# Performance work log

Measured on AMD Instinct MI355X. Metric: run time of the kernel, lower is better.

Reference implementation:

```python
import jax, jax.numpy as jnp
import numpy as np

B, S, D, H, F = 2, 2048, 1024, 16, 4096
HD = D // H
EPS = 1e-5


def setup_inputs() -> dict:
    key = jax.random.key(0)
    ks = jax.random.split(key, 12)
    sc = 0.02
    inp = {
        "feature": jax.random.normal(ks[0], (B, S, D), jnp.float32),
        "src_key_padding_mask": jnp.ones((B, S), bool),
        # torch Linear weights stored as [in, out] (already transposed)
        "wq": jax.random.normal(ks[1], (D, D), jnp.float32) * sc,
        "bq": jnp.zeros((D,), jnp.float32),
        "wk": jax.random.normal(ks[2], (D, D), jnp.float32) * sc,
        "bk": jnp.zeros((D,), jnp.float32),
        "wv": jax.random.normal(ks[3], (D, D), jnp.float32) * sc,
        "bv": jnp.zeros((D,), jnp.float32),
        "wo": jax.random.normal(ks[4], (D, D), jnp.float32) * sc,
        "bo": jnp.zeros((D,), jnp.float32),
        "ln1_g": jnp.ones((D,), jnp.float32),
        "ln1_b": jnp.zeros((D,), jnp.float32),
        "ln2_g": jnp.ones((D,), jnp.float32),
        "ln2_b": jnp.zeros((D,), jnp.float32),
        "w1": jax.random.normal(ks[5], (D, F), jnp.float32) * sc,
        "b1": jnp.zeros((F,), jnp.float32),
        "w2": jax.random.normal(ks[6], (F, D), jnp.float32) * sc,
        "b2": jnp.zeros((D,), jnp.float32),
    }
    return inp


def _layer_norm(x, g, b):
    mu = jnp.mean(x, axis=-1, keepdims=True)
    var = jnp.mean(jnp.square(x - mu), axis=-1, keepdims=True)
    return (x - mu) * jax.lax.rsqrt(var + EPS) * g + b


def _encoder_layer(feature, san_mask, wq, bq, wk, bk, wv, bv, wo, bo,
                   ln1_g, ln1_b, ln2_g, ln2_b, w1, b1, w2, b2):
    # pre-norm (_forward_prenorm), dropout = 0 (eval)
    residual = feature
    x = _layer_norm(feature, ln1_g, ln1_b)
    q = (x @ wq + bq).reshape(B, S, H, HD)
    k = (x @ wk + bk).reshape(B, S, H, HD)
    v = (x @ wv + bv).reshape(B, S, H, HD)
    scale = jnp.float32(np.sqrt(HD))
    scores = jnp.einsum('bihd,bjhd->bhij', q, k) / scale  # [B,H,S,S]
    neg_inf = jnp.finfo(scores.dtype).min
    if san_mask is not None:
        scores = jnp.where(san_mask[:, None, :, :], scores, neg_inf)
    attw = jax.nn.softmax(scores, axis=-1)
    cvec = jnp.einsum('bhij,bjhd->bihd', attw, v).reshape(B, S, D)
    feature = cvec @ wo + bo + residual
    residual = feature
    x = _layer_norm(feature, ln2_g, ln2_b)
    x = jax.nn.gelu(x @ w1 + b1, approximate=False) @ w2 + b2
    return x + residual


def reference(feature, src_key_padding_mask, wq, bq, wk, bk, wv, bv, wo, bo,
              ln1_g, ln1_b, ln2_g, ln2_b, w1, b1, w2, b2):
    # make_san_mask: pad_mask [B,S] -> [B,S(q),S(k)] (no causal mask)
    san_mask = jnp.broadcast_to(src_key_padding_mask[:, None, :], (B, S, S))
    return _encoder_layer(feature, san_mask, wq, bq, wk, bk, wv, bv, wo, bo,
                          ln1_g, ln1_b, ln2_g, ln2_b, w1, b1, w2, b2)
```

## Files before the change

kernel.cpp:

```cpp
#include <hip/hip_runtime.h>
#include <hip/hip_bf16.h>
#include <math.h>

#define BB   2
#define SS   2048
#define DD   1024
#define HH   16
#define HDIM 64
#define FF   4096

typedef __hip_bfloat16 bf16_t;
typedef short s8v __attribute__((ext_vector_type(8)));
typedef float f4v __attribute__((ext_vector_type(4)));

#define PSTRIDE 4194304

__device__ inline unsigned bfr(float x) {
    unsigned u = __float_as_uint(x);
    return (u + 0x7fffu + ((u >> 16) & 1u)) >> 16;
}
__device__ inline unsigned bfpack(float lo, float hi) {
    return bfr(lo) | (bfr(hi) << 16);
}
__device__ inline float bflo(unsigned u) { return __uint_as_float(u << 16); }
__device__ inline float bfhi(unsigned u) { return __uint_as_float(u & 0xffff0000u); }
__device__ inline void gload16(const void* g, void* l) {
    __builtin_amdgcn_global_load_lds(
        (const __attribute__((address_space(1))) void*)g,
        (__attribute__((address_space(3))) void*)l, 16, 0, 0);
}

__global__ __launch_bounds__(256) void wtrans_all(
    const float* __restrict__ wq, const float* __restrict__ wk,
    const float* __restrict__ wv, const float* __restrict__ wo,
    const float* __restrict__ w1, const float* __restrict__ w2,
    bf16_t* __restrict__ dqkv, bf16_t* __restrict__ dwo,
    bf16_t* __restrict__ dw1, bf16_t* __restrict__ dw2) {
    __shared__ float tile[32][33];
    int id = blockIdx.x;
    const float* src; bf16_t* dst; int K, N, n0, k0;
    if (id < 4096) {
        int seg = id >> 10, r = id & 1023;
        K = 1024; N = 1024; n0 = (r & 31) * 32; k0 = (r >> 5) * 32;
        if (seg == 0)      { src = wq; dst = dqkv; }
        else if (seg == 1) { src = wk; dst = dqkv + 1024 * 1024; }
        else if (seg == 2) { src = wv; dst = dqkv + 2 * 1024 * 1024; }
        else               { src = wo; dst = dwo; }
    } else if (id < 8192) {
        int r = id - 4096;
        K = 1024; N = 4096; n0 = (r & 127) * 32; k0 = (r >> 7) * 32;
        src = w1; dst = dw1;
    } else {
        int r = id - 8192;
        K = 4096; N = 1024; n0 = (r & 31) * 32; k0 = (r >> 5) * 32;
        src = w2; dst = dw2;
    }
    int tx = threadIdx.x, ty = threadIdx.y;
#pragma unroll
    for (int i = 0; i < 4; i++)
        tile[ty * 4 + i][tx] = src[(size_t)(k0 + ty * 4 + i) * N + n0 + tx];
    __syncthreads();
#pragma unroll
    for (int i = 0; i < 4; i++) {
        unsigned short h = (unsigned short)bfr(tile[tx][ty * 4 + i]);
        *(unsigned short*)&dst[(size_t)(n0 + ty * 4 + i) * K + k0 + tx] = h;
    }
}

__global__ __launch_bounds__(256) void ln_k(const float* __restrict__ x,
                                            const float* __restrict__ gam,
                                            const float* __restrict__ bet,
                                            bf16_t* __restrict__ out) {
    int row = blockIdx.x, t = threadIdx.x;
    const float4 v = *(const float4*)&x[(size_t)row * DD + t * 4];
    float s  = v.x + v.y + v.z + v.w;
    float s2 = v.x * v.x + v.y * v.y + v.z * v.z + v.w * v.w;
#pragma unroll
    for (int off = 1; off < 64; off <<= 1) {
        s  += __shfl_xor(s, off);
        s2 += __shfl_xor(s2, off);
    }
    __shared__ float sb[8];
    int w = t >> 6, lane = t & 63;
    if (lane == 0) { sb[w] = s; sb[4 + w] = s2; }
    __syncthreads();
    s  = sb[0] + sb[1] + sb[2] + sb[3];
    s2 = sb[4] + sb[5] + sb[6] + sb[7];
    float mu  = s * (1.f / DD);
    float var = s2 * (1.f / DD) - mu * mu;
    float rs  = rsqrtf(var + 1e-5f);
    float4 gv = *(const float4*)&gam[t * 4];
    float4 bv = *(const float4*)&bet[t * 4];
    float o0 = (v.x - mu) * rs * gv.x + bv.x;
    float o1 = (v.y - mu) * rs * gv.y + bv.y;
    float o2 = (v.z - mu) * rs * gv.z + bv.z;
    float o3 = (v.w - mu) * rs * gv.w + bv.w;
    uint2 uu; uu.x = bfpack(o0, o1); uu.y = bfpack(o2, o3);
    *(uint2*)&out[(size_t)row * DD + t * 4] = uu;
}

template <int MODE, int SPLITS, int SWIZ>
__global__ __launch_bounds__(256, 2) void gemm_bt(
    const bf16_t* __restrict__ A, const bf16_t* __restrict__ Bt,
    int M, int N, int K,
    const float* __restrict__ bias0, const float* __restrict__ bias1,
    const float* __restrict__ bias2, const float* __restrict__ resid,
    float* __restrict__ outF,
    bf16_t* __restrict__ o0, bf16_t* __restrict__ o1, bf16_t* __restrict__ o2) {
    __shared__ bf16_t As[128 * 64];
    __shared__ bf16_t Bs[128 * 64];
    const int t = threadIdx.x;
    const int lane = t & 63, w = t >> 6;
    const int c = lane & 15, g = lane >> 4;
    const int wm = w & 1, wn = w >> 1;

    int bx, by, z;
    if (SWIZ == 0) { bx = blockIdx.x; by = blockIdx.y; z = blockIdx.z; }
    else if (SWIZ == 1) {
        int b = blockIdx.x, xcd = b & 7, j = b >> 3;
        by = xcd * 4 + (j & 3); bx = j >> 2; z = 0;
    } else {
        int b = blockIdx.x, xcd = b & 7, j = b >> 3;
        z = xcd >> 1; by = (xcd & 1) * 16 + (j & 15); bx = j >> 4;
    }
    const int m0 = by * 128, n0 = bx * 128;

    f4v acc[4][4];
#pragma unroll
    for (int i = 0; i < 4; i++)
#pragma unroll
        for (int j = 0; j < 4; j++)
#pragma unroll
            for (int r = 0; r < 4; r++) acc[i][j][r] = 0.f;

    const int row0 = t >> 3;
    const int kk   = (((t & 7) ^ (row0 & 7)) << 3);
    const bf16_t* ga = A  + (size_t)(m0 + row0) * K + kk;
    const bf16_t* gb = Bt + (size_t)(n0 + row0) * K + kk;

    const int fs0 = ((g)     ^ (c & 7)) * 8;
    const int fs1 = ((4 + g) ^ (c & 7)) * 8;
    int kbeg = 0, kend = K;
    if (MODE == 3) { kbeg = z * (K / SPLITS); kend = kbeg + (K / SPLITS); }

    for (int k0 = kbeg; k0 < kend; k0 += 64) {
        __syncthreads();
#pragma unroll
        for (int p = 0; p < 4; p++) {
            gload16(ga + k0 + (size_t)(32 * p) * K, &As[p * 2048 + t * 8]);
            gload16(gb + k0 + (size_t)(32 * p) * K, &Bs[p * 2048 + t * 8]);
        }
        __syncthreads();
#pragma unroll
        for (int kh = 0; kh < 2; kh++) {
            const int fs = kh ? fs1 : fs0;
            s8v af[4], bfg[4];
#pragma unroll
            for (int mi = 0; mi < 4; mi++)
                af[mi] = *(const s8v*)&As[(wm * 64 + mi * 16 + c) * 64 + fs];
#pragma unroll
            for (int ni = 0; ni < 4; ni++)
                bfg[ni] = *(const s8v*)&Bs[(wn * 64 + ni * 16 + c) * 64 + fs];
#pragma unroll
            for (int mi = 0; mi < 4; mi++)
#pragma unroll
                for (int ni = 0; ni < 4; ni++)
                    acc[mi][ni] = __builtin_amdgcn_mfma_f32_16x16x32_bf16(
                        af[mi], bfg[ni], acc[mi][ni], 0, 0, 0);
        }
    }

#pragma unroll
    for (int mi = 0; mi < 4; mi++) {
        int m = m0 + wm * 64 + mi * 16 + g * 4;
#pragma unroll
        for (int ni = 0; ni < 4; ni++) {
            int n = n0 + wn * 64 + ni * 16 + c;
            if (MODE == 0) {
                int seg = n >> 10, n2 = n & 1023;
                const float* bp = (seg == 0) ? bias0 : (seg == 1 ? bias1 : bias2);
                float bias = bp[n2];
                int h = n2 >> 6, hd = n2 & 63;
                int b = m >> 11, s = m & 2047;
                if (seg == 2) {
                    uint2 uu;
                    uu.x = bfpack(acc[mi][ni][0] + bias, acc[mi][ni][1] + bias);
                    uu.y = bfpack(acc[mi][ni][2] + bias, acc[mi][ni][3] + bias);
                    *(uint2*)&o2[((size_t)((b * HH + h) * HDIM + hd)) * SS + s] = uu;
                } else {
                    bf16_t* op = (seg == 0) ? o0 : o1;
                    float sc = (seg == 0) ? 0.18033688011112042f : 1.0f;
                    size_t base = ((size_t)(b * HH + h) * SS + s) * HDIM + hd;
#pragma unroll
                    for (int r = 0; r < 4; r++)
                        *(unsigned short*)&op[base + (size_t)r * HDIM] =
                            (unsigned short)bfr((acc[mi][ni][r] + bias) * sc);
                }
            } else if (MODE == 1) {
                float bias = bias0[n];
#pragma unroll
                for (int r = 0; r < 4; r++) {
                    size_t off = (size_t)(m + r) * N + n;
                    outF[off] = acc[mi][ni][r] + bias + resid[off];
                }
            } else if (MODE == 2) {
                float bias = bias0[n];
#pragma unroll
                for (int r = 0; r < 4; r++) {
                    float xg = acc[mi][ni][r] + bias;
                    float y  = 0.5f * xg * (1.0f + erff(xg * 0.70710678118654752f));
                    *(unsigned short*)&o0[(size_t)(m + r) * N + n] =
                        (unsigned short)bfr(y);
                }
            } else {
                bf16_t* po = o0 + (size_t)z * PSTRIDE;
#pragma unroll
                for (int r = 0; r < 4; r++)
                    *(unsigned short*)&po[(size_t)(m + r) * N + n] =
                        (unsigned short)bfr(acc[mi][ni][r]);
            }
        }
    }
}

__global__ __launch_bounds__(256) void combine_ln(
    const bf16_t* __restrict__ P, const float* __restrict__ bias,
    const float* __restrict__ resid, float* __restrict__ feat2,
    const float* __restrict__ gam, const float* __restrict__ bet,
    bf16_t* __restrict__ out) {
    int row = blockIdx.x, t = threadIdx.x;
    size_t off = (size_t)row * DD + t * 4;
    float4 bi = *(const float4*)&bias[t * 4];
    float4 rz = *(const float4*)&resid[off];
    float4 v;
    v.x = bi.x + rz.x; v.y = bi.y + rz.y; v.z = bi.z + rz.z; v.w = bi.w + rz.w;
#pragma unroll
    for (int p = 0; p < 4; p++) {
        uint2 u = *(const uint2*)&P[(size_t)p * PSTRIDE + off];
        v.x += bflo(u.x); v.y += bfhi(u.x); v.z += bflo(u.y); v.w += bfhi(u.y);
    }
    *(float4*)&feat2[off] = v;
    float s  = v.x + v.y + v.z + v.w;
    float s2 = v.x * v.x + v.y * v.y + v.z * v.z + v.w * v.w;
#pragma unroll
    for (int o = 1; o < 64; o <<= 1) {
        s  += __shfl_xor(s, o);
        s2 += __shfl_xor(s2, o);
    }
    __shared__ float sb[8];
    int w = t >> 6, lane = t & 63;
    if (lane == 0) { sb[w] = s; sb[4 + w] = s2; }
    __syncthreads();
    s  = sb[0] + sb[1] + sb[2] + sb[3];
    s2 = sb[4] + sb[5] + sb[6] + sb[7];
    float mu  = s * (1.f / DD);
    float var = s2 * (1.f / DD) - mu * mu;
    float rs  = rsqrtf(var + 1e-5f);
    float4 gv = *(const float4*)&gam[t * 4];
    float4 bv = *(const float4*)&bet[t * 4];
    float o0 = (v.x - mu) * rs * gv.x + bv.x;
    float o1 = (v.y - mu) * rs * gv.y + bv.y;
    float o2 = (v.z - mu) * rs * gv.z + bv.z;
    float o3 = (v.w - mu) * rs * gv.w + bv.w;
    uint2 uu; uu.x = bfpack(o0, o1); uu.y = bfpack(o2, o3);
    *(uint2*)&out[off] = uu;
}

__global__ __launch_bounds__(256) void combine_out(
    const bf16_t* __restrict__ P, const float* __restrict__ bias,
    const float* __restrict__ resid, float* __restrict__ out) {
    int idx = blockIdx.x * 256 + threadIdx.x;
    size_t off = (size_t)idx * 4;
    int n = (idx & 255) * 4;
    float4 bi = *(const float4*)&bias[n];
    float4 rz = *(const float4*)&resid[off];
    float4 v;
    v.x = bi.x + rz.x; v.y = bi.y + rz.y; v.z = bi.z + rz.z; v.w = bi.w + rz.w;
#pragma unroll
    for (int p = 0; p < 4; p++) {
        uint2 u = *(const uint2*)&P[(size_t)p * PSTRIDE + off];
        v.x += bflo(u.x); v.y += bfhi(u.x); v.z += bflo(u.y); v.w += bfhi(u.y);
    }
    *(float4*)&out[off] = v;
}

__global__ __launch_bounds__(256, 4) void flash_attn(
    const bf16_t* __restrict__ qb, const bf16_t* __restrict__ kb,
    const bf16_t* __restrict__ vbt, bf16_t* __restrict__ Op,
    float* __restrict__ Lp) {
    __shared__ char smem[34816];
    bf16_t* QP = (bf16_t*)smem;
    bf16_t* Ks = (bf16_t*)(smem + 18432);
    bf16_t* Vt = (bf16_t*)(smem + 26624);
    const int t = threadIdx.x, lane = t & 63, w = t >> 6;
    const int c = lane & 15, g = lane >> 4;
    const int bh = blockIdx.x, s0 = blockIdx.y * 128, z = blockIdx.z;
    const bf16_t* qg = qb  + (size_t)bh * SS * HDIM;

    {
        int row = t >> 3, col = (t & 7) << 3;
#pragma unroll
        for (int r2 = 0; r2 < 4; r2++) {
            int rr = row + 32 * r2;
            *(s8v*)&QP[rr * 72 + col] =
                *(const s8v*)&qg[(size_t)(s0 + rr) * HDIM + col];
        }
    }
    __syncthreads();
    s8v bq[2][2];
#pragma unroll
    for (int ni = 0; ni < 2; ni++)
#pragma unroll
        for (int kh = 0; kh < 2; kh++)
            bq[ni][kh] = *(const s8v*)&QP[(w * 32 + ni * 16 + c) * 72 + kh * 32 + g * 8];
    bf16_t* Ps = QP + w * (32 * 72);

    const int pr1 = t >> 3,          pc1 = (t & 7) ^ (pr1 & 7);
    const int pr2 = (t >> 3) + 32,   pc2 = (t & 7) ^ (pr2 & 7);
    const bf16_t* kR1 = kb + (size_t)bh * SS * HDIM + ((size_t)z * 1024 + pr1) * HDIM + pc1 * 8;
    const bf16_t* kR2 = kb + (size_t)bh * SS * HDIM + ((size_t)z * 1024 + pr2) * HDIM + pc2 * 8;
    const bf16_t* vR1 = vbt + ((size_t)bh * HDIM + pr1) * SS + z * 1024 + pc1 * 8;
    const bf16_t* vR2 = vbt + ((size_t)bh * HDIM + pr2) * SS + z * 1024 + pc2 * 8;

    float lsum[2] = {0.f, 0.f};
    f4v oacc[4][2];
#pragma unroll
    for (int i = 0; i < 4; i++)
#pragma unroll
        for (int j = 0; j < 2; j++)
#pragma unroll
            for (int r = 0; r < 4; r++) oacc[i][j][r] = 0.f;

    for (int kt = 0; kt < 16; kt++) {
        __syncthreads();
        gload16(kR1, &Ks[t * 8]);
        gload16(kR2, &Ks[(t + 256) * 8]);
        gload16(vR1, &Vt[t * 8]);
        gload16(vR2, &Vt[(t + 256) * 8]);
        kR1 += 64 * HDIM; kR2 += 64 * HDIM; vR1 += 64; vR2 += 64;
        __syncthreads();

        f4v sacc[4][2];
#pragma unroll
        for (int i = 0; i < 4; i++)
#pragma unroll
            for (int j = 0; j < 2; j++)
#pragma unroll
                for (int r = 0; r < 4; r++) sacc[i][j][r] = 0.f;
#pragma unroll
        for (int kh = 0; kh < 2; kh++)
#pragma unroll
            for (int mi = 0; mi < 4; mi++) {
                s8v ak = *(const s8v*)&Ks[((mi * 16 + c) * 8 + ((kh * 4 + g) ^ (c & 7))) * 8];
#pragma unroll
                for (int ni = 0; ni < 2; ni++)
                    sacc[mi][ni] = __builtin_amdgcn_mfma_f32_16x16x32_bf16(
                        ak, bq[ni][kh], sacc[mi][ni], 0, 0, 0);
            }

#pragma unroll
        for (int ni = 0; ni < 2; ni++) {
#pragma unroll
            for (int mi = 0; mi < 4; mi++) {
                float p0 = __builtin_amdgcn_exp2f(sacc[mi][ni][0]);
                float p1 = __builtin_amdgcn_exp2f(sacc[mi][ni][1]);
                float p2 = __builtin_amdgcn_exp2f(sacc[mi][ni][2]);
                float p3 = __builtin_amdgcn_exp2f(sacc[mi][ni][3]);
                lsum[ni] += (p0 + p1) + (p2 + p3);
                uint2 uu;
                uu.x = __builtin_amdgcn_perm(__float_as_uint(p1), __float_as_uint(p0), 0x07060302u);
                uu.y = __builtin_amdgcn_perm(__float_as_uint(p3), __float_as_uint(p2), 0x07060302u);
                *(uint2*)&Ps[(ni * 16 + c) * 72 + mi * 16 + g * 4] = uu;
            }
        }

#pragma unroll
        for (int ks = 0; ks < 2; ks++) {
            s8v pb[2];
#pragma unroll
            for (int ni = 0; ni < 2; ni++)
                pb[ni] = *(const s8v*)&Ps[(ni * 16 + c) * 72 + ks * 32 + g * 8];
#pragma unroll
            for (int mi = 0; mi < 4; mi++) {
                s8v av = *(const s8v*)&Vt[((mi * 16 + c) * 8 + ((ks * 4 + g) ^ (c & 7))) * 8];
#pragma unroll
                for (int ni = 0; ni < 2; ni++)
                    oacc[mi][ni] = __builtin_amdgcn_mfma_f32_16x16x32_bf16(
                        av, pb[ni], oacc[mi][ni], 0, 0, 0);
            }
        }
    }

    int b = bh >> 4, h = bh & 15;
#pragma unroll
    for (int ni = 0; ni < 2; ni++) {
        lsum[ni] += __shfl_xor(lsum[ni], 16);
        lsum[ni] += __shfl_xor(lsum[ni], 32);
        int q = s0 + w * 32 + ni * 16 + c;
        if (g == 0)
            Lp[(size_t)z * (32 * SS) + bh * SS + q] = lsum[ni];
#pragma unroll
        for (int mi = 0; mi < 4; mi++) {
            uint2 uu;
            uu.x = bfpack(oacc[mi][ni][0], oacc[mi][ni][1]);
            uu.y = bfpack(oacc[mi][ni][2], oacc[mi][ni][3]);
            *(uint2*)&Op[(size_t)z * (4096 * 1024) +
                         ((size_t)(b * SS + q)) * DD + h * HDIM + mi * 16 + g * 4] = uu;
        }
    }
}

__global__ __launch_bounds__(256) void attn_combine(
    const bf16_t* __restrict__ Op, const float* __restrict__ Lp,
    bf16_t* __restrict__ ctx) {
    int idx = blockIdx.x * 256 + threadIdx.x;
    int row = idx >> 8;
    int col = (idx & 255) * 4;
    int b = row >> 11, q = row & 2047, h = col >> 6;
    size_t o = (size_t)row * DD + col;
    uint2 u0 = *(const uint2*)&Op[o];
    uint2 u1 = *(const uint2*)&Op[(size_t)(4096 * 1024) + o];
    int lb = (b * HH + h) * SS + q;
    float inv = 1.f / (Lp[lb] + Lp[32 * SS + lb]);
    float a0 = bflo(u0.x) + bflo(u1.x);
    float a1 = bfhi(u0.x) + bfhi(u1.x);
    float a2 = bflo(u0.y) + bflo(u1.y);
    float a3 = bfhi(u0.y) + bfhi(u1.y);
    uint2 uu;
    uu.x = bfpack(a0 * inv, a1 * inv);
    uu.y = bfpack(a2 * inv, a3 * inv);
    *(uint2*)&ctx[o] = uu;
}

extern "C" void kernel_launch(void* const* d_in, const int* in_sizes, int n_in,
                              void* d_out, int out_size, void* d_ws, size_t ws_size,
                              hipStream_t stream) {
    (void)in_sizes; (void)n_in; (void)out_size; (void)ws_size;
    const float* feature = (const float*)d_in[0];
    const float* wq = (const float*)d_in[2];  const float* bq = (const float*)d_in[3];
    const float* wk = (const float*)d_in[4];  const float* bk = (const float*)d_in[5];
    const float* wv = (const float*)d_in[6];  const float* bv = (const float*)d_in[7];
    const float* wo = (const float*)d_in[8];  const float* bo = (const float*)d_in[9];
    const float* g1 = (const float*)d_in[10]; const float* be1 = (const float*)d_in[11];
    const float* g2 = (const float*)d_in[12]; const float* be2 = (const float*)d_in[13];
    const float* w1 = (const float*)d_in[14]; const float* b1  = (const float*)d_in[15];
    const float* w2 = (const float*)d_in[16]; const float* b2  = (const float*)d_in[17];
    float* outp = (float*)d_out;

    char* ws = (char*)d_ws;
    bf16_t* wqkvT = (bf16_t*)(ws);
    bf16_t* woT   = (bf16_t*)(ws + 6291456);
    bf16_t* w1T   = (bf16_t*)(ws + 8388608);
    bf16_t* w2T   = (bf16_t*)(ws + 16777216);
    bf16_t* xln1  = (bf16_t*)(ws + 25165824);
    bf16_t* qbuf  = (bf16_t*)(ws + 33554432);
    bf16_t* kbuf  = (bf16_t*)(ws + 41943040);
    bf16_t* vbuf  = (bf16_t*)(ws + 50331648);
    bf16_t* ctxb  = (bf16_t*)(ws + 58720256);
    bf16_t* Opart = (bf16_t*)(ws + 67108864);
    float*  feat2 = (float*) (ws + 67108864);
    float*  Lpart = (float*) (ws + 83886080);
    bf16_t* xln2  = (bf16_t*)(ws + 83886080);
    bf16_t* hbuf  = (bf16_t*)(ws + 92274688);
    bf16_t* Pwo   = (bf16_t*)(ws + 92274688);
    bf16_t* Pw2   = (bf16_t*)(ws + 33554432);

    wtrans_all<<<12288, dim3(32, 8), 0, stream>>>(wq, wk, wv, wo, w1, w2,
                                                  wqkvT, woT, w1T, w2T);

    ln_k<<<4096, 256, 0, stream>>>(feature, g1, be1, xln1);

    gemm_bt<0, 1, 1><<<768, 256, 0, stream>>>(
        xln1, wqkvT, 4096, 3072, 1024, bq, bk, bv,
        nullptr, nullptr, qbuf, kbuf, vbuf);

    flash_attn<<<dim3(32, 16, 2), 256, 0, stream>>>(qbuf, kbuf, vbuf, Opart, Lpart);
    attn_combine<<<4096, 256, 0, stream>>>(Opart, Lpart, ctxb);

    gemm_bt<3, 4, 2><<<1024, 256, 0, stream>>>(
        ctxb, woT, 4096, 1024, 1024, nullptr, nullptr, nullptr,
        nullptr, nullptr, Pwo, nullptr, nullptr);
    combine_ln<<<4096, 256, 0, stream>>>(Pwo, bo, feature, feat2, g2, be2, xln2);

    gemm_bt<2, 1, 1><<<1024, 256, 0, stream>>>(
        xln2, w1T, 4096, 4096, 1024, b1, nullptr, nullptr,
        nullptr, nullptr, hbuf, nullptr, nullptr);

    gemm_bt<3, 4, 2><<<1024, 256, 0, stream>>>(
        hbuf, w2T, 4096, 1024, 4096, nullptr, nullptr, nullptr,
        nullptr, nullptr, Pw2, nullptr, nullptr);
    combine_out<<<4096, 256, 0, stream>>>(Pw2, b2, feat2, outp);
}
```

Baseline: 343.1 us.

## Merge weight transpose with LN1 and restructure flash attention warp split

Folds the first layer norm into the weight-transpose kernel so both run as one launch. Flash attention now splits keys three ways instead of two and divides each key tile across warp pairs. Each warp holds 64 queries against 32 keys, and the two partial outputs are reduced through shared memory. The aim is more blocks in flight, fewer launches and more reuse of each Q fragment, at the cost of more registers (occupancy hint drops from 4 to 3), an in-block reduction, and an extra partial buffer to combine.

```diff
diff --git a/kernel.cpp b/kernel.cpp
--- a/kernel.cpp
+++ b/kernel.cpp
@@ -30,73 +30,73 @@
         (__attribute__((address_space(3))) void*)l, 16, 0, 0);
 }
 
-__global__ __launch_bounds__(256) void wtrans_all(
+__global__ __launch_bounds__(256) void prep(
     const float* __restrict__ wq, const float* __restrict__ wk,
     const float* __restrict__ wv, const float* __restrict__ wo,
     const float* __restrict__ w1, const float* __restrict__ w2,
     bf16_t* __restrict__ dqkv, bf16_t* __restrict__ dwo,
-    bf16_t* __restrict__ dw1, bf16_t* __restrict__ dw2) {
+    bf16_t* __restrict__ dw1, bf16_t* __restrict__ dw2,
+    const float* __restrict__ x, const float* __restrict__ gam,
+    const float* __restrict__ bet, bf16_t* __restrict__ lnout) {
     __shared__ float tile[32][33];
     int id = blockIdx.x;
-    const float* src; bf16_t* dst; int K, N, n0, k0;
-    if (id < 4096) {
-        int seg = id >> 10, r = id & 1023;
-        K = 1024; N = 1024; n0 = (r & 31) * 32; k0 = (r >> 5) * 32;
-        if (seg == 0)      { src = wq; dst = dqkv; }
-        else if (seg == 1) { src = wk; dst = dqkv + 1024 * 1024; }
-        else if (seg == 2) { src = wv; dst = dqkv + 2 * 1024 * 1024; }
-        else               { src = wo; dst = dwo; }
-    } else if (id < 8192) {
-        int r = id - 4096;
-        K = 1024; N = 4096; n0 = (r & 127) * 32; k0 = (r >> 7) * 32;
-        src = w1; dst = dw1;
+    int t = threadIdx.x;
+    if (id < 12288) {
+        const float* src; bf16_t* dst; int K, N, n0, k0;
+        if (id < 4096) {
+            int seg = id >> 10, r = id & 1023;
+            K = 1024; N = 1024; n0 = (r & 31) * 32; k0 = (r >> 5) * 32;
+            if (seg == 0)      { src = wq; dst = dqkv; }
+            else if (seg == 1) { src = wk; dst = dqkv + 1024 * 1024; }
+            else if (seg == 2) { src = wv; dst = dqkv + 2 * 1024 * 1024; }
+            else               { src = wo; dst = dwo; }
+        } else if (id < 8192) {
+            int r = id - 4096;
+            K = 1024; N = 4096; n0 = (r & 127) * 32; k0 = (r >> 7) * 32;
+            src = w1; dst = dw1;
+        } else {
+            int r = id - 8192;
+            K = 4096; N = 1024; n0 = (r & 31) * 32; k0 = (r >> 5) * 32;
+            src = w2; dst = dw2;
+        }
+        int tx = t & 31, ty = t >> 5;
+#pragma unroll
+        for (int i = 0; i < 4; i++)
+            tile[ty * 4 + i][tx] = src[(size_t)(k0 + ty * 4 + i) * N + n0 + tx];
+        __syncthreads();
+#pragma unroll
+        for (int i = 0; i < 4; i++) {
+            unsigned short h = (unsigned short)bfr(tile[tx][ty * 4 + i]);
+            *(unsigned short*)&dst[(size_t)(n0 + ty * 4 + i) * K + k0 + tx] = h;
+        }
     } else {
-        int r = id - 8192;
-        K = 4096; N = 1024; n0 = (r & 31) * 32; k0 = (r >> 5) * 32;
-        src = w2; dst = dw2;
-    }
-    int tx = threadIdx.x, ty = threadIdx.y;
-#pragma unroll
-    for (int i = 0; i < 4; i++)
-        tile[ty * 4 + i][tx] = src[(size_t)(k0 + ty * 4 + i) * N + n0 + tx];
-    __syncthreads();
-#pragma unroll
-    for (int i = 0; i < 4; i++) {
-        unsigned short h = (unsigned short)bfr(tile[tx][ty * 4 + i]);
-        *(unsigned short*)&dst[(size_t)(n0 + ty * 4 + i) * K + k0 + tx] = h;
-    }
-}
-
-__global__ __launch_bounds__(256) void ln_k(const float* __restrict__ x,
-                                            const float* __restrict__ gam,
-                                            const float* __restrict__ bet,
-                                            bf16_t* __restrict__ out) {
-    int row = blockIdx.x, t = threadIdx.x;
-    const float4 v = *(const float4*)&x[(size_t)row * DD + t * 4];
-    float s  = v.x + v.y + v.z + v.w;
-    float s2 = v.x * v.x + v.y * v.y + v.z * v.z + v.w * v.w;
-#pragma unroll
-    for (int off = 1; off < 64; off <<= 1) {
-        s  += __shfl_xor(s, off);
-        s2 += __shfl_xor(s2, off);
-    }
-    __shared__ float sb[8];
-    int w = t >> 6, lane = t & 63;
-    if (lane == 0) { sb[w] = s; sb[4 + w] = s2; }
-    __syncthreads();
-    s  = sb[0] + sb[1] + sb[2] + sb[3];
-    s2 = sb[4] + sb[5] + sb[6] + sb[7];
-    float mu  = s * (1.f / DD);
-    float var = s2 * (1.f / DD) - mu * mu;
-    float rs  = rsqrtf(var + 1e-5f);
-    float4 gv = *(const float4*)&gam[t * 4];
-    float4 bv = *(const float4*)&bet[t * 4];
-    float o0 = (v.x - mu) * rs * gv.x + bv.x;
-    float o1 = (v.y - mu) * rs * gv.y + bv.y;
-    float o2 = (v.z - mu) * rs * gv.z + bv.z;
-    float o3 = (v.w - mu) * rs * gv.w + bv.w;
-    uint2 uu; uu.x = bfpack(o0, o1); uu.y = bfpack(o2, o3);
-    *(uint2*)&out[(size_t)row * DD + t * 4] = uu;
+        int row = id - 12288;
+        float* sb = &tile[0][0];
+        const float4 v = *(const float4*)&x[(size_t)row * DD + t * 4];
+        float s  = v.x + v.y + v.z + v.w;
+        float s2 = v.x * v.x + v.y * v.y + v.z * v.z + v.w * v.w;
+#pragma unroll
+        for (int off = 1; off < 64; off <<= 1) {
+            s  += __shfl_xor(s, off);
+            s2 += __shfl_xor(s2, off);
+        }
+        int w = t >> 6, lane = t & 63;
+        if (lane == 0) { sb[w] = s; sb[4 + w] = s2; }
+        __syncthreads();
+        s  = sb[0] + sb[1] + sb[2] + sb[3];
+        s2 = sb[4] + sb[5] + sb[6] + sb[7];
+        float mu  = s * (1.f / DD);
+        float var = s2 * (1.f / DD) - mu * mu;
+        float rs  = rsqrtf(var + 1e-5f);
+        float4 gv = *(const float4*)&gam[t * 4];
+        float4 bv = *(const float4*)&bet[t * 4];
+        float o0 = (v.x - mu) * rs * gv.x + bv.x;
+        float o1 = (v.y - mu) * rs * gv.y + bv.y;
+        float o2 = (v.z - mu) * rs * gv.z + bv.z;
+        float o3 = (v.w - mu) * rs * gv.w + bv.w;
+        uint2 uu; uu.x = bfpack(o0, o1); uu.y = bfpack(o2, o3);
+        *(uint2*)&lnout[(size_t)row * DD + t * 4] = uu;
+    }
 }
 
 template <int MODE, int SPLITS, int SWIZ>
@@ -284,18 +284,22 @@
     *(float4*)&out[off] = v;
 }
 
-__global__ __launch_bounds__(256, 4) void flash_attn(
+__global__ __launch_bounds__(256, 3) void flash_attn(
     const bf16_t* __restrict__ qb, const bf16_t* __restrict__ kb,
     const bf16_t* __restrict__ vbt, bf16_t* __restrict__ Op,
     float* __restrict__ Lp) {
-    __shared__ char smem[34816];
+    __shared__ char smem[36864];
     bf16_t* QP = (bf16_t*)smem;
-    bf16_t* Ks = (bf16_t*)(smem + 18432);
-    bf16_t* Vt = (bf16_t*)(smem + 26624);
+    bf16_t* Ks = (bf16_t*)(smem + 20480);
+    bf16_t* Vt = (bf16_t*)(smem + 28672);
+    float*  Rr = (float*)smem;
+    float*  Lr = (float*)(smem + 34816);
     const int t = threadIdx.x, lane = t & 63, w = t >> 6;
     const int c = lane & 15, g = lane >> 4;
+    const int kw = w & 1, qw = w >> 1;
     const int bh = blockIdx.x, s0 = blockIdx.y * 128, z = blockIdx.z;
-    const bf16_t* qg = qb  + (size_t)bh * SS * HDIM;
+    const int kt0 = z * 11, kt1 = (z == 2) ? 32 : (z * 11 + 11);
+    const bf16_t* qg = qb + (size_t)bh * SS * HDIM;
 
     {
         int row = t >> 3, col = (t & 7) << 3;
@@ -307,31 +311,32 @@
         }
     }
     __syncthreads();
-    s8v bq[2][2];
-#pragma unroll
-    for (int ni = 0; ni < 2; ni++)
+    s8v bq[4][2];
+#pragma unroll
+    for (int ni = 0; ni < 4; ni++)
 #pragma unroll
         for (int kh = 0; kh < 2; kh++)
-            bq[ni][kh] = *(const s8v*)&QP[(w * 32 + ni * 16 + c) * 72 + kh * 32 + g * 8];
-    bf16_t* Ps = QP + w * (32 * 72);
+            bq[ni][kh] = *(const s8v*)&QP[(qw * 64 + ni * 16 + c) * 72 + kh * 32 + g * 8];
+    __syncthreads();
+    bf16_t* Ps = (bf16_t*)smem + w * 2560;
 
     const int pr1 = t >> 3,          pc1 = (t & 7) ^ (pr1 & 7);
     const int pr2 = (t >> 3) + 32,   pc2 = (t & 7) ^ (pr2 & 7);
-    const bf16_t* kR1 = kb + (size_t)bh * SS * HDIM + ((size_t)z * 1024 + pr1) * HDIM + pc1 * 8;
-    const bf16_t* kR2 = kb + (size_t)bh * SS * HDIM + ((size_t)z * 1024 + pr2) * HDIM + pc2 * 8;
-    const bf16_t* vR1 = vbt + ((size_t)bh * HDIM + pr1) * SS + z * 1024 + pc1 * 8;
-    const bf16_t* vR2 = vbt + ((size_t)bh * HDIM + pr2) * SS + z * 1024 + pc2 * 8;
-
-    float lsum[2] = {0.f, 0.f};
-    f4v oacc[4][2];
+    const bf16_t* kR1 = kb + (size_t)bh * SS * HDIM + ((size_t)kt0 * 64 + pr1) * HDIM + pc1 * 8;
+    const bf16_t* kR2 = kb + (size_t)bh * SS * HDIM + ((size_t)kt0 * 64 + pr2) * HDIM + pc2 * 8;
+    const bf16_t* vR1 = vbt + ((size_t)bh * HDIM + pr1) * SS + kt0 * 64 + pc1 * 8;
+    const bf16_t* vR2 = vbt + ((size_t)bh * HDIM + pr2) * SS + kt0 * 64 + pc2 * 8;
+
+    float lsum[4] = {0.f, 0.f, 0.f, 0.f};
+    f4v oacc[4][4];
 #pragma unroll
     for (int i = 0; i < 4; i++)
 #pragma unroll
-        for (int j = 0; j < 2; j++)
+        for (int j = 0; j < 4; j++)
 #pragma unroll
             for (int r = 0; r < 4; r++) oacc[i][j][r] = 0.f;
 
-    for (int kt = 0; kt < 16; kt++) {
+    for (int kt = kt0; kt < kt1; kt++) {
         __syncthreads();
         gload16(kR1, &Ks[t * 8]);
         gload16(kR2, &Ks[(t + 256) * 8]);
@@ -340,28 +345,29 @@
         kR1 += 64 * HDIM; kR2 += 64 * HDIM; vR1 += 64; vR2 += 64;
         __syncthreads();
 
-        f4v sacc[4][2];
-#pragma unroll
-        for (int i = 0; i < 4; i++)
-#pragma unroll
-            for (int j = 0; j < 2; j++)
+        f4v sacc[2][4];
+#pragma unroll
+        for (int i = 0; i < 2; i++)
+#pragma unroll
+            for (int j = 0; j < 4; j++)
 #pragma unroll
                 for (int r = 0; r < 4; r++) sacc[i][j][r] = 0.f;
 #pragma unroll
         for (int kh = 0; kh < 2; kh++)
 #pragma unroll
-            for (int mi = 0; mi < 4; mi++) {
-                s8v ak = *(const s8v*)&Ks[((mi * 16 + c) * 8 + ((kh * 4 + g) ^ (c & 7))) * 8];
-#pragma unroll
-                for (int ni = 0; ni < 2; ni++)
+            for (int mi = 0; mi < 2; mi++) {
+                s8v ak = *(const s8v*)&Ks[(kw * 32 + mi * 16 + c) * 64 +
+                                          (((kh * 4 + g) ^ (c & 7)) * 8)];
+#pragma unroll
+                for (int ni = 0; ni < 4; ni++)
                     sacc[mi][ni] = __builtin_amdgcn_mfma_f32_16x16x32_bf16(
                         ak, bq[ni][kh], sacc[mi][ni], 0, 0, 0);
             }
 
 #pragma unroll
-        for (int ni = 0; ni < 2; ni++) {
-#pragma unroll
-            for (int mi = 0; mi < 4; mi++) {
+        for (int ni = 0; ni < 4; ni++)
+#pragma unroll
+            for (int mi = 0; mi < 2; mi++) {
                 float p0 = __builtin_amdgcn_exp2f(sacc[mi][ni][0]);
                 float p1 = __builtin_amdgcn_exp2f(sacc[mi][ni][1]);
                 float p2 = __builtin_amdgcn_exp2f(sacc[mi][ni][2]);
@@ -370,42 +376,66 @@
                 uint2 uu;
                 uu.x = __builtin_amdgcn_perm(__float_as_uint(p1), __float_as_uint(p0), 0x07060302u);
                 uu.y = __builtin_amdgcn_perm(__float_as_uint(p3), __float_as_uint(p2), 0x07060302u);
-                *(uint2*)&Ps[(ni * 16 + c) * 72 + mi * 16 + g * 4] = uu;
+                *(uint2*)&Ps[(ni * 16 + c) * 40 + mi * 16 + g * 4] = uu;
             }
-        }
-
-#pragma unroll
-        for (int ks = 0; ks < 2; ks++) {
-            s8v pb[2];
-#pragma unroll
-            for (int ni = 0; ni < 2; ni++)
-                pb[ni] = *(const s8v*)&Ps[(ni * 16 + c) * 72 + ks * 32 + g * 8];
-#pragma unroll
-            for (int mi = 0; mi < 4; mi++) {
-                s8v av = *(const s8v*)&Vt[((mi * 16 + c) * 8 + ((ks * 4 + g) ^ (c & 7))) * 8];
-#pragma unroll
-                for (int ni = 0; ni < 2; ni++)
-                    oacc[mi][ni] = __builtin_amdgcn_mfma_f32_16x16x32_bf16(
-                        av, pb[ni], oacc[mi][ni], 0, 0, 0);
-            }
-        }
-    }
-
-    int b = bh >> 4, h = bh & 15;
-#pragma unroll
-    for (int ni = 0; ni < 2; ni++) {
+
+        s8v pb[4];
+#pragma unroll
+        for (int ni = 0; ni < 4; ni++)
+            pb[ni] = *(const s8v*)&Ps[(ni * 16 + c) * 40 + g * 8];
+#pragma unroll
+        for (int mi = 0; mi < 4; mi++) {
+            s8v av = *(const s8v*)&Vt[(mi * 16 + c) * 64 +
+                                      (((kw * 4 + g) ^ (c & 7)) * 8)];
+#pragma unroll
+            for (int ni = 0; ni < 4; ni++)
+                oacc[mi][ni] = __builtin_amdgcn_mfma_f32_16x16x32_bf16(
+                    av, pb[ni], oacc[mi][ni], 0, 0, 0);
+        }
+    }
+
+#pragma unroll
+    for (int ni = 0; ni < 4; ni++) {
         lsum[ni] += __shfl_xor(lsum[ni], 16);
         lsum[ni] += __shfl_xor(lsum[ni], 32);
-        int q = s0 + w * 32 + ni * 16 + c;
+    }
+
+    __syncthreads();
+    if (kw == 1) {
+        float* R = Rr + qw * (64 * 68);
+#pragma unroll
+        for (int mi = 0; mi < 4; mi++)
+#pragma unroll
+            for (int ni = 0; ni < 4; ni++) {
+                float4 fv;
+                fv.x = oacc[mi][ni][0]; fv.y = oacc[mi][ni][1];
+                fv.z = oacc[mi][ni][2]; fv.w = oacc[mi][ni][3];
+                *(float4*)&R[(ni * 16 + c) * 68 + mi * 16 + g * 4] = fv;
+            }
         if (g == 0)
-            Lp[(size_t)z * (32 * SS) + bh * SS + q] = lsum[ni];
-#pragma unroll
-        for (int mi = 0; mi < 4; mi++) {
-            uint2 uu;
-            uu.x = bfpack(oacc[mi][ni][0], oacc[mi][ni][1]);
-            uu.y = bfpack(oacc[mi][ni][2], oacc[mi][ni][3]);
-            *(uint2*)&Op[(size_t)z * (4096 * 1024) +
-                         ((size_t)(b * SS + q)) * DD + h * HDIM + mi * 16 + g * 4] = uu;
+#pragma unroll
+            for (int ni = 0; ni < 4; ni++)
+                Lr[qw * 64 + ni * 16 + c] = lsum[ni];
+    }
+    __syncthreads();
+    if (kw == 0) {
+        float* R = Rr + qw * (64 * 68);
+        int b = bh >> 4, h = bh & 15;
+#pragma unroll
+        for (int ni = 0; ni < 4; ni++) {
+            float ltot = lsum[ni] + Lr[qw * 64 + ni * 16 + c];
+            int q = s0 + qw * 64 + ni * 16 + c;
+            if (g == 0)
+                Lp[(size_t)z * (32 * SS) + bh * SS + q] = ltot;
+#pragma unroll
+            for (int mi = 0; mi < 4; mi++) {
+                float4 rv = *(const float4*)&R[(ni * 16 + c) * 68 + mi * 16 + g * 4];
+                uint2 uu;
+                uu.x = bfpack(oacc[mi][ni][0] + rv.x, oacc[mi][ni][1] + rv.y);
+                uu.y = bfpack(oacc[mi][ni][2] + rv.z, oacc[mi][ni][3] + rv.w);
+                *(uint2*)&Op[(size_t)z * (4096 * 1024) +
+                             ((size_t)(b * SS + q)) * DD + h * HDIM + mi * 16 + g * 4] = uu;
+            }
         }
     }
 }
@@ -418,14 +448,14 @@
     int col = (idx & 255) * 4;
     int b = row >> 11, q = row & 2047, h = col >> 6;
     size_t o = (size_t)row * DD + col;
-    uint2 u0 = *(const uint2*)&Op[o];
-    uint2 u1 = *(const uint2*)&Op[(size_t)(4096 * 1024) + o];
     int lb = (b * HH + h) * SS + q;
-    float inv = 1.f / (Lp[lb] + Lp[32 * SS + lb]);
-    float a0 = bflo(u0.x) + bflo(u1.x);
-    float a1 = bfhi(u0.x) + bfhi(u1.x);
-    float a2 = bflo(u0.y) + bflo(u1.y);
-    float a3 = bfhi(u0.y) + bfhi(u1.y);
+    float inv = 1.f / (Lp[lb] + Lp[32 * SS + lb] + Lp[2 * 32 * SS + lb]);
+    float a0 = 0.f, a1 = 0.f, a2 = 0.f, a3 = 0.f;
+#pragma unroll
+    for (int z = 0; z < 3; z++) {
+        uint2 u = *(const uint2*)&Op[(size_t)z * (4096 * 1024) + o];
+        a0 += bflo(u.x); a1 += bfhi(u.x); a2 += bflo(u.y); a3 += bfhi(u.y);
+    }
     uint2 uu;
     uu.x = bfpack(a0 * inv, a1 * inv);
     uu.y = bfpack(a2 * inv, a3 * inv);
@@ -457,24 +487,23 @@
     bf16_t* kbuf  = (bf16_t*)(ws + 41943040);
     bf16_t* vbuf  = (bf16_t*)(ws + 50331648);
     bf16_t* ctxb  = (bf16_t*)(ws + 58720256);
-    bf16_t* Opart = (bf16_t*)(ws + 67108864);
     float*  feat2 = (float*) (ws + 67108864);
     float*  Lpart = (float*) (ws + 83886080);
     bf16_t* xln2  = (bf16_t*)(ws + 83886080);
     bf16_t* hbuf  = (bf16_t*)(ws + 92274688);
+    bf16_t* Opart = (bf16_t*)(ws + 92274688);
     bf16_t* Pwo   = (bf16_t*)(ws + 92274688);
     bf16_t* Pw2   = (bf16_t*)(ws + 33554432);
 
-    wtrans_all<<<12288, dim3(32, 8), 0, stream>>>(wq, wk, wv, wo, w1, w2,
-                                                  wqkvT, woT, w1T, w2T);
-
-    ln_k<<<4096, 256, 0, stream>>>(feature, g1, be1, xln1);
+    prep<<<16384, 256, 0, stream>>>(wq, wk, wv, wo, w1, w2,
+                                    wqkvT, woT, w1T, w2T,
+                                    feature, g1, be1, xln1);
 
     gemm_bt<0, 1, 1><<<768, 256, 0, stream>>>(
         xln1, wqkvT, 4096, 3072, 1024, bq, bk, bv,
         nullptr, nullptr, qbuf, kbuf, vbuf);
 
-    flash_attn<<<dim3(32, 16, 2), 256, 0, stream>>>(qbuf, kbuf, vbuf, Opart, Lpart);
+    flash_attn<<<dim3(32, 16, 3), 256, 0, stream>>>(qbuf, kbuf, vbuf, Opart, Lpart);
     attn_combine<<<4096, 256, 0, stream>>>(Opart, Lpart, ctxb);
 
     gemm_bt<3, 4, 2><<<1024, 256, 0, stream>>>(
```

Result: slower. 350.3 us (+2.1%).

## Merge weight transpose with layernorm and register-prefetch K/V tiles in flash attention

Applied to the files above, without the earlier changes.

Merges the weight transpose/cast kernel and the first layernorm into one launch by giving the layernorm rows their own block range. In flash attention, Q fragments are now loaded straight from global memory instead of being staged through LDS, and K/V tiles are prefetched into registers one iteration ahead. The register tile is written to LDS at the top of each step, replacing the direct global-to-LDS loads, so global latency can overlap with the MFMA work. The Opart buffer also moves to a different workspace offset, and the prefetch adds register pressure in a kernel launched with an occupancy target of 4.

```diff
diff --git a/kernel.cpp b/kernel.cpp
--- a/kernel.cpp
+++ b/kernel.cpp
@@ -30,73 +30,73 @@
         (__attribute__((address_space(3))) void*)l, 16, 0, 0);
 }
 
-__global__ __launch_bounds__(256) void wtrans_all(
+__global__ __launch_bounds__(256) void prep(
     const float* __restrict__ wq, const float* __restrict__ wk,
     const float* __restrict__ wv, const float* __restrict__ wo,
     const float* __restrict__ w1, const float* __restrict__ w2,
     bf16_t* __restrict__ dqkv, bf16_t* __restrict__ dwo,
-    bf16_t* __restrict__ dw1, bf16_t* __restrict__ dw2) {
+    bf16_t* __restrict__ dw1, bf16_t* __restrict__ dw2,
+    const float* __restrict__ x, const float* __restrict__ gam,
+    const float* __restrict__ bet, bf16_t* __restrict__ lnout) {
     __shared__ float tile[32][33];
     int id = blockIdx.x;
-    const float* src; bf16_t* dst; int K, N, n0, k0;
-    if (id < 4096) {
-        int seg = id >> 10, r = id & 1023;
-        K = 1024; N = 1024; n0 = (r & 31) * 32; k0 = (r >> 5) * 32;
-        if (seg == 0)      { src = wq; dst = dqkv; }
-        else if (seg == 1) { src = wk; dst = dqkv + 1024 * 1024; }
-        else if (seg == 2) { src = wv; dst = dqkv + 2 * 1024 * 1024; }
-        else               { src = wo; dst = dwo; }
-    } else if (id < 8192) {
-        int r = id - 4096;
-        K = 1024; N = 4096; n0 = (r & 127) * 32; k0 = (r >> 7) * 32;
-        src = w1; dst = dw1;
+    int t = threadIdx.x;
+    if (id < 12288) {
+        const float* src; bf16_t* dst; int K, N, n0, k0;
+        if (id < 4096) {
+            int seg = id >> 10, r = id & 1023;
+            K = 1024; N = 1024; n0 = (r & 31) * 32; k0 = (r >> 5) * 32;
+            if (seg == 0)      { src = wq; dst = dqkv; }
+            else if (seg == 1) { src = wk; dst = dqkv + 1024 * 1024; }
+            else if (seg == 2) { src = wv; dst = dqkv + 2 * 1024 * 1024; }
+            else               { src = wo; dst = dwo; }
+        } else if (id < 8192) {
+            int r = id - 4096;
+            K = 1024; N = 4096; n0 = (r & 127) * 32; k0 = (r >> 7) * 32;
+            src = w1; dst = dw1;
+        } else {
+            int r = id - 8192;
+            K = 4096; N = 1024; n0 = (r & 31) * 32; k0 = (r >> 5) * 32;
+            src = w2; dst = dw2;
+        }
+        int tx = t & 31, ty = t >> 5;
+#pragma unroll
+        for (int i = 0; i < 4; i++)
+            tile[ty * 4 + i][tx] = src[(size_t)(k0 + ty * 4 + i) * N + n0 + tx];
+        __syncthreads();
+#pragma unroll
+        for (int i = 0; i < 4; i++) {
+            unsigned short h = (unsigned short)bfr(tile[tx][ty * 4 + i]);
+            *(unsigned short*)&dst[(size_t)(n0 + ty * 4 + i) * K + k0 + tx] = h;
+        }
     } else {
-        int r = id - 8192;
-        K = 4096; N = 1024; n0 = (r & 31) * 32; k0 = (r >> 5) * 32;
-        src = w2; dst = dw2;
-    }
-    int tx = threadIdx.x, ty = threadIdx.y;
-#pragma unroll
-    for (int i = 0; i < 4; i++)
-        tile[ty * 4 + i][tx] = src[(size_t)(k0 + ty * 4 + i) * N + n0 + tx];
-    __syncthreads();
-#pragma unroll
-    for (int i = 0; i < 4; i++) {
-        unsigned short h = (unsigned short)bfr(tile[tx][ty * 4 + i]);
-        *(unsigned short*)&dst[(size_t)(n0 + ty * 4 + i) * K + k0 + tx] = h;
-    }
-}
-
-__global__ __launch_bounds__(256) void ln_k(const float* __restrict__ x,
-                                            const float* __restrict__ gam,
-                                            const float* __restrict__ bet,
-                                            bf16_t* __restrict__ out) {
-    int row = blockIdx.x, t = threadIdx.x;
-    const float4 v = *(const float4*)&x[(size_t)row * DD + t * 4];
-    float s  = v.x + v.y + v.z + v.w;
-    float s2 = v.x * v.x + v.y * v.y + v.z * v.z + v.w * v.w;
-#pragma unroll
-    for (int off = 1; off < 64; off <<= 1) {
-        s  += __shfl_xor(s, off);
-        s2 += __shfl_xor(s2, off);
-    }
-    __shared__ float sb[8];
-    int w = t >> 6, lane = t & 63;
-    if (lane == 0) { sb[w] = s; sb[4 + w] = s2; }
-    __syncthreads();
-    s  = sb[0] + sb[1] + sb[2] + sb[3];
-    s2 = sb[4] + sb[5] + sb[6] + sb[7];
-    float mu  = s * (1.f / DD);
-    float var = s2 * (1.f / DD) - mu * mu;
-    float rs  = rsqrtf(var + 1e-5f);
-    float4 gv = *(const float4*)&gam[t * 4];
-    float4 bv = *(const float4*)&bet[t * 4];
-    float o0 = (v.x - mu) * rs * gv.x + bv.x;
-    float o1 = (v.y - mu) * rs * gv.y + bv.y;
-    float o2 = (v.z - mu) * rs * gv.z + bv.z;
-    float o3 = (v.w - mu) * rs * gv.w + bv.w;
-    uint2 uu; uu.x = bfpack(o0, o1); uu.y = bfpack(o2, o3);
-    *(uint2*)&out[(size_t)row * DD + t * 4] = uu;
+        int row = id - 12288;
+        float* sb = &tile[0][0];
+        const float4 v = *(const float4*)&x[(size_t)row * DD + t * 4];
+        float s  = v.x + v.y + v.z + v.w;
+        float s2 = v.x * v.x + v.y * v.y + v.z * v.z + v.w * v.w;
+#pragma unroll
+        for (int off = 1; off < 64; off <<= 1) {
+            s  += __shfl_xor(s, off);
+            s2 += __shfl_xor(s2, off);
+        }
+        int w = t >> 6, lane = t & 63;
+        if (lane == 0) { sb[w] = s; sb[4 + w] = s2; }
+        __syncthreads();
+        s  = sb[0] + sb[1] + sb[2] + sb[3];
+        s2 = sb[4] + sb[5] + sb[6] + sb[7];
+        float mu  = s * (1.f / DD);
+        float var = s2 * (1.f / DD) - mu * mu;
+        float rs  = rsqrtf(var + 1e-5f);
+        float4 gv = *(const float4*)&gam[t * 4];
+        float4 bv = *(const float4*)&bet[t * 4];
+        float o0 = (v.x - mu) * rs * gv.x + bv.x;
+        float o1 = (v.y - mu) * rs * gv.y + bv.y;
+        float o2 = (v.z - mu) * rs * gv.z + bv.z;
+        float o3 = (v.w - mu) * rs * gv.w + bv.w;
+        uint2 uu; uu.x = bfpack(o0, o1); uu.y = bfpack(o2, o3);
+        *(uint2*)&lnout[(size_t)row * DD + t * 4] = uu;
+    }
 }
 
 template <int MODE, int SPLITS, int SWIZ>
@@ -289,31 +289,22 @@
     const bf16_t* __restrict__ vbt, bf16_t* __restrict__ Op,
     float* __restrict__ Lp) {
     __shared__ char smem[34816];
-    bf16_t* QP = (bf16_t*)smem;
-    bf16_t* Ks = (bf16_t*)(smem + 18432);
-    bf16_t* Vt = (bf16_t*)(smem + 26624);
+    bf16_t* Ps0 = (bf16_t*)smem;
+    bf16_t* Ks  = (bf16_t*)(smem + 18432);
+    bf16_t* Vt  = (bf16_t*)(smem + 26624);
     const int t = threadIdx.x, lane = t & 63, w = t >> 6;
     const int c = lane & 15, g = lane >> 4;
     const int bh = blockIdx.x, s0 = blockIdx.y * 128, z = blockIdx.z;
-    const bf16_t* qg = qb  + (size_t)bh * SS * HDIM;
-
-    {
-        int row = t >> 3, col = (t & 7) << 3;
-#pragma unroll
-        for (int r2 = 0; r2 < 4; r2++) {
-            int rr = row + 32 * r2;
-            *(s8v*)&QP[rr * 72 + col] =
-                *(const s8v*)&qg[(size_t)(s0 + rr) * HDIM + col];
-        }
-    }
-    __syncthreads();
+    const bf16_t* qg = qb + (size_t)bh * SS * HDIM;
+    bf16_t* Ps = Ps0 + w * (32 * 72);
+
     s8v bq[2][2];
 #pragma unroll
     for (int ni = 0; ni < 2; ni++)
 #pragma unroll
         for (int kh = 0; kh < 2; kh++)
-            bq[ni][kh] = *(const s8v*)&QP[(w * 32 + ni * 16 + c) * 72 + kh * 32 + g * 8];
-    bf16_t* Ps = QP + w * (32 * 72);
+            bq[ni][kh] = *(const s8v*)&qg[(size_t)(s0 + w * 32 + ni * 16 + c) * HDIM +
+                                          kh * 32 + g * 8];
 
     const int pr1 = t >> 3,          pc1 = (t & 7) ^ (pr1 & 7);
     const int pr2 = (t >> 3) + 32,   pc2 = (t & 7) ^ (pr2 & 7);
@@ -322,6 +313,9 @@
     const bf16_t* vR1 = vbt + ((size_t)bh * HDIM + pr1) * SS + z * 1024 + pc1 * 8;
     const bf16_t* vR2 = vbt + ((size_t)bh * HDIM + pr2) * SS + z * 1024 + pc2 * 8;
 
+    s8v pk1 = *(const s8v*)kR1, pk2 = *(const s8v*)kR2;
+    s8v pv1 = *(const s8v*)vR1, pv2 = *(const s8v*)vR2;
+
     float lsum[2] = {0.f, 0.f};
     f4v oacc[4][2];
 #pragma unroll
@@ -333,12 +327,16 @@
 
     for (int kt = 0; kt < 16; kt++) {
         __syncthreads();
-        gload16(kR1, &Ks[t * 8]);
-        gload16(kR2, &Ks[(t + 256) * 8]);
-        gload16(vR1, &Vt[t * 8]);
-        gload16(vR2, &Vt[(t + 256) * 8]);
-        kR1 += 64 * HDIM; kR2 += 64 * HDIM; vR1 += 64; vR2 += 64;
-        __syncthreads();
+        *(s8v*)&Ks[t * 8]         = pk1;
+        *(s8v*)&Ks[(t + 256) * 8] = pk2;
+        *(s8v*)&Vt[t * 8]         = pv1;
+        *(s8v*)&Vt[(t + 256) * 8] = pv2;
+        __syncthreads();
+        if (kt < 15) {
+            kR1 += 64 * HDIM; kR2 += 64 * HDIM; vR1 += 64; vR2 += 64;
+            pk1 = *(const s8v*)kR1; pk2 = *(const s8v*)kR2;
+            pv1 = *(const s8v*)vR1; pv2 = *(const s8v*)vR2;
+        }
 
         f4v sacc[4][2];
 #pragma unroll
@@ -457,18 +455,17 @@
     bf16_t* kbuf  = (bf16_t*)(ws + 41943040);
     bf16_t* vbuf  = (bf16_t*)(ws + 50331648);
     bf16_t* ctxb  = (bf16_t*)(ws + 58720256);
-    bf16_t* Opart = (bf16_t*)(ws + 67108864);
     float*  feat2 = (float*) (ws + 67108864);
     float*  Lpart = (float*) (ws + 83886080);
     bf16_t* xln2  = (bf16_t*)(ws + 83886080);
     bf16_t* hbuf  = (bf16_t*)(ws + 92274688);
+    bf16_t* Opart = (bf16_t*)(ws + 92274688);
     bf16_t* Pwo   = (bf16_t*)(ws + 92274688);
     bf16_t* Pw2   = (bf16_t*)(ws + 33554432);
 
-    wtrans_all<<<12288, dim3(32, 8), 0, stream>>>(wq, wk, wv, wo, w1, w2,
-                                                  wqkvT, woT, w1T, w2T);
-
-    ln_k<<<4096, 256, 0, stream>>>(feature, g1, be1, xln1);
+    prep<<<16384, 256, 0, stream>>>(wq, wk, wv, wo, w1, w2,
+                                    wqkvT, woT, w1T, w2T,
+                                    feature, g1, be1, xln1);
 
     gemm_bt<0, 1, 1><<<768, 256, 0, stream>>>(
         xln1, wqkvT, 4096, 3072, 1024, bq, bk, bv,
```

Result: faster. 335.2 us (-2.3%).
